# Performance work log

Measured on AMD Instinct MI355X. Metric: run time of the kernel, lower is better.

Reference implementation:

```python
import jax, jax.numpy as jnp
import numpy as np

B, C, H, W = 8, 512, 64, 128
K = 19          # num_classes
BH, BW = 2, 4   # bin_size
N = BH * BW     # bin_num
CI = C // 2     # feat_inner


def setup_inputs() -> dict:
    ks = jax.random.split(jax.random.key(0), 10)
    def nrm(k, shape, s=0.02):
        return jax.random.normal(k, shape, jnp.float32) * s
    return {
        "x": jax.random.normal(ks[0], (B, C, H, W), jnp.float32),
        "conv_cam_w": nrm(ks[1], (K, C)),
        "conv_cam_b": jnp.zeros((K,), jnp.float32),
        "gcn_w1": nrm(ks[2], (N, N), 0.1),
        "gcn_a": jnp.full((N,), 0.25, jnp.float32),
        "gcn_w2": nrm(ks[3], (C, C)),
        "fuse_w": nrm(ks[4], (1, N), 0.1),
        "fuse_b": jnp.zeros((1,), jnp.float32),
        "relu_a": jnp.full((1,), 0.25, jnp.float32),
        "q_w": nrm(ks[5], (CI, C)),
        "q_b": jnp.zeros((CI,), jnp.float32),
        "k_w": nrm(ks[6], (CI, C)),
        "k_b": jnp.zeros((CI,), jnp.float32),
        "v_w": nrm(ks[7], (CI, C)),
        "v_b": jnp.zeros((CI,), jnp.float32),
        "out_w": nrm(ks[8], (C, CI)),
        "bn_gamma": jnp.ones((C,), jnp.float32),
        "bn_beta": jnp.zeros((C,), jnp.float32),
        "out_a": jnp.full((C,), 0.25, jnp.float32),
    }


def _prelu(x, a):
    return jnp.maximum(x, 0) + a * jnp.minimum(x, 0)


def _split(t):
    # [b, cc, H, W] -> [b, N, rh*rw, cc]  (patch_split)
    b, cc = t.shape[0], t.shape[1]
    rh, rw = H // BH, W // BW
    t = t.reshape(b, cc, BH, rh, BW, rw).transpose(0, 2, 4, 3, 5, 1)
    return t.reshape(b, N, rh * rw, cc)


def _caam(x, conv_cam_w, conv_cam_b, gcn_w1, gcn_a, gcn_w2, fuse_w, fuse_b,
          relu_a, q_w, q_b, k_w, k_b, v_w, v_b, out_w, bn_gamma, bn_beta, out_a):
    b = x.shape[0]
    rh, rw = H // BH, W // BW
    # CAM (1x1 conv) + adaptive avg pool to bins + sigmoid
    cam = jnp.einsum('bchw,kc->bkhw', x, conv_cam_w) + conv_cam_b[None, :, None, None]
    cls_score = jax.nn.sigmoid(cam.reshape(b, K, BH, rh, BW, rw).mean((3, 5)))  # [b,K,BH,BW]
    cam_p = _split(cam)   # [b,N,P,K]
    x_p = _split(x)       # [b,N,P,C]
    bin_conf = cls_score.reshape(b, K, N).transpose(0, 2, 1)[..., None]  # [b,N,K,1]
    pix_conf = jax.nn.softmax(cam_p, axis=2)
    local = jnp.einsum('bnpk,bnpc->bnkc', pix_conf, x_p) * bin_conf  # [b,N,K,C]
    # GCN: conv1 over bin dim, PReLU(residual), Linear over channels
    t = jnp.einsum('nm,bmkc->bnkc', gcn_w1, local)
    t = _prelu(t + local, gcn_a[None, :, None, None])
    local = jnp.einsum('bnkc,dc->bnkd', t, gcn_w2)
    # fuse bins -> single global descriptor, PReLU(1)
    glob = jnp.einsum('on,bnkc->bokc', fuse_w, local) + fuse_b[None, :, None, None]  # [b,1,K,C]
    glob = _prelu(glob[:, 0], relu_a[0])  # [b,K,C]
    # QKV attention over bins (key/value over K class slots)
    q = jnp.einsum('bnpc,ic->bnpi', x_p, q_w) + q_b       # [b,N,P,CI]
    key = jnp.einsum('bnkc,ic->bnki', local, k_w) + k_b   # [b,N,K,CI]
    val = jnp.einsum('bkc,ic->bki', glob, v_w) + v_b      # [b,K,CI] (shared across bins)
    aff = jax.nn.softmax(jnp.einsum('bnpi,bnki->bnpk', q, key), axis=-1)
    out = jnp.einsum('bnpk,bki->bnpi', aff, val)          # [b,N,P,CI]
    # patch_recover -> [b,CI,H,W]
    out = out.reshape(b, BH, BW, rh, rw, CI).transpose(0, 5, 1, 3, 2, 4).reshape(b, CI, H, W)
    # conv_out: 1x1 conv (no bias) + BatchNorm2d (batch stats) + PReLU(C)
    y = jnp.einsum('bihw,ci->bchw', out, out_w)
    mu = y.mean((0, 2, 3), keepdims=True)
    var = y.var((0, 2, 3), keepdims=True)
    y = (y - mu) * jax.lax.rsqrt(var + 1e-5)
    y = y * bn_gamma[None, :, None, None] + bn_beta[None, :, None, None]
    y = _prelu(y, out_a[None, :, None, None])
    return x + y


def reference(x, conv_cam_w, conv_cam_b, gcn_w1, gcn_a, gcn_w2, fuse_w, fuse_b,
              relu_a, q_w, q_b, k_w, k_b, v_w, v_b, out_w, bn_gamma, bn_beta, out_a):
    return _caam(x, conv_cam_w, conv_cam_b, gcn_w1, gcn_a, gcn_w2, fuse_w, fuse_b,
                 relu_a, q_w, q_b, k_w, k_b, v_w, v_b, out_w, bn_gamma, bn_beta, out_a)
```

## Files before the change

### kernel.cpp

```cpp
#include <hip/hip_runtime.h>
#include <cstdint>
#include <cstddef>

#define B_ 8
#define C_ 512
#define H_ 64
#define W_ 128
#define HW_ 8192
#define K_ 19
#define N_ 8
#define P_ 1024
#define CI_ 256

typedef unsigned short u16;
typedef unsigned int u32;
typedef __attribute__((ext_vector_type(8))) short bf16x8;
typedef __attribute__((ext_vector_type(4))) float f32x4;

__device__ __forceinline__ u16 f2bf(float f) {
  u32 u = __float_as_uint(f);
  u32 r = (u + 0x7FFFu + ((u >> 16) & 1u)) >> 16;
  return (u16)r;
}
__device__ __forceinline__ float bf2f(u16 h) {
  return __uint_as_float(((u32)h) << 16);
}

__device__ __forceinline__ float blockSum256(float v, float* red4) {
#pragma unroll
  for (int o = 32; o > 0; o >>= 1) v += __shfl_down(v, o, 64);
  __syncthreads();
  if ((threadIdx.x & 63) == 0) red4[threadIdx.x >> 6] = v;
  __syncthreads();
  return red4[0] + red4[1] + red4[2] + red4[3];
}

__device__ __forceinline__ float blockMax256(float v, float* red4) {
#pragma unroll
  for (int o = 32; o > 0; o >>= 1) v = fmaxf(v, __shfl_down(v, o, 64));
  __syncthreads();
  if ((threadIdx.x & 63) == 0) red4[threadIdx.x >> 6] = v;
  __syncthreads();
  return fmaxf(fmaxf(red4[0], red4[1]), fmaxf(red4[2], red4[3]));
}

__device__ __forceinline__ void cvt4(const float* __restrict__ s, u16* __restrict__ d, int i) {
  float4 v = *(const float4*)&s[(size_t)i * 4];
  ushort4 o;
  o.x = f2bf(v.x); o.y = f2bf(v.y); o.z = f2bf(v.z); o.w = f2bf(v.w);
  *(ushort4*)&d[(size_t)i * 4] = o;
}

__global__ __launch_bounds__(256) void prep_kernel(const float* __restrict__ qw,
                                                   const float* __restrict__ ow,
                                                   const float* __restrict__ kw,
                                                   const float* __restrict__ gw2,
                                                   const float* __restrict__ camw,
                                                   u16* __restrict__ qwbf,
                                                   u16* __restrict__ owbf,
                                                   u16* __restrict__ kwbf,
                                                   u16* __restrict__ gw2bf,
                                                   u16* __restrict__ camwbf,
                                                   float* __restrict__ sums,
                                                   float* __restrict__ tpad) {
  int bid = blockIdx.x, tid = threadIdx.x;
  if (bid < 128) {
    cvt4(qw, qwbf, bid * 256 + tid);
  } else if (bid < 256) {
    cvt4(ow, owbf, (bid - 128) * 256 + tid);
  } else if (bid < 384) {
    cvt4(kw, kwbf, (bid - 256) * 256 + tid);
  } else if (bid < 640) {
    cvt4(gw2, gw2bf, (bid - 384) * 256 + tid);
  } else if (bid < 656) {
    int i = (bid - 640) * 256 + tid;
    if (i * 4 < K_ * C_) {
      cvt4(camw, camwbf, i);
    } else {
      ushort4 z; z.x = 0; z.y = 0; z.z = 0; z.w = 0;
      *(ushort4*)&camwbf[(size_t)i * 4] = z;
    }
  } else if (bid == 656) {
    float4 z; z.x = 0.f; z.y = 0.f; z.z = 0.f; z.w = 0.f;
    *(float4*)&sums[tid * 4] = z;
  } else {
    int i = (bid - 657) * 256 + tid;
    float4 z; z.x = 0.f; z.y = 0.f; z.z = 0.f; z.w = 0.f;
    *(float4*)&tpad[(size_t)i * 4] = z;
  }
}

__global__ __launch_bounds__(256) void xpose_kernel(const float* __restrict__ x,
                                                    u16* __restrict__ xt) {
  __shared__ float tile[64][65];
  int bid = blockIdx.x;
  int hw0 = (bid & 127) << 6;
  int c0 = ((bid >> 7) & 7) << 6;
  int b = bid >> 10;
  int tid = threadIdx.x;
  int r = tid >> 4;
  int col4 = (tid & 15) << 2;
  const float* xb = x + ((size_t)b * C_ + c0) * HW_ + hw0;
#pragma unroll
  for (int it = 0; it < 4; it++) {
    int rr = r + it * 16;
    float4 v = *(const float4*)&xb[(size_t)rr * HW_ + col4];
    tile[rr][col4 + 0] = v.x;
    tile[rr][col4 + 1] = v.y;
    tile[rr][col4 + 2] = v.z;
    tile[rr][col4 + 3] = v.w;
  }
  __syncthreads();
  u16* xo = xt + ((size_t)b * HW_ + hw0) * C_ + c0;
#pragma unroll
  for (int it = 0; it < 4; it++) {
    int hwr = r + it * 16;
    ushort4 o;
    o.x = f2bf(tile[col4 + 0][hwr]);
    o.y = f2bf(tile[col4 + 1][hwr]);
    o.z = f2bf(tile[col4 + 2][hwr]);
    o.w = f2bf(tile[col4 + 3][hwr]);
    *(ushort4*)&xo[(size_t)hwr * C_ + col4] = o;
  }
}

__global__ __launch_bounds__(256) void gemm_cam_kernel(const u16* __restrict__ A,
                                                       const u16* __restrict__ Bw,
                                                       const float* __restrict__ bias,
                                                       float* __restrict__ cam) {
  __shared__ u16 As[128 * 72];
  __shared__ u16 Bs[32 * 72];
  int b = blockIdx.y;
  int m0 = blockIdx.x * 128;
  int tid = threadIdx.x;
  int wave = tid >> 6, lane = tid & 63;
  int wm = wave * 32;
  int quad = lane >> 4, l16 = lane & 15;
  const u16* Ab = A + (size_t)b * HW_ * C_ + (size_t)m0 * C_;
  f32x4 acc[2][2] = {};
  int sr = tid >> 3;
  int sk = (tid & 7) * 8;
  for (int k0 = 0; k0 < C_; k0 += 64) {
    __syncthreads();
#pragma unroll
    for (int it = 0; it < 4; it++) {
      int r = sr + it * 32;
      *(uint4*)&As[r * 72 + sk] = *(const uint4*)&Ab[(size_t)r * C_ + k0 + sk];
    }
    { int r = tid >> 3;
      *(uint4*)&Bs[r * 72 + sk] = *(const uint4*)&Bw[(size_t)r * C_ + k0 + sk]; }
    __syncthreads();
#pragma unroll
    for (int kk = 0; kk < 2; kk++) {
      bf16x8 af[2], bfv[2];
#pragma unroll
      for (int t = 0; t < 2; t++) {
        af[t] = *(const bf16x8*)&As[(wm + t * 16 + l16) * 72 + kk * 32 + quad * 8];
        bfv[t] = *(const bf16x8*)&Bs[(t * 16 + l16) * 72 + kk * 32 + quad * 8];
      }
#pragma unroll
      for (int tm = 0; tm < 2; tm++)
#pragma unroll
        for (int tn = 0; tn < 2; tn++)
          acc[tm][tn] = __builtin_amdgcn_mfma_f32_16x16x32_bf16(af[tm], bfv[tn], acc[tm][tn], 0, 0, 0);
    }
  }
  float* C = cam + (size_t)b * K_ * HW_;
#pragma unroll
  for (int tm = 0; tm < 2; tm++) {
    int mm = m0 + wm + tm * 16 + quad * 4;
#pragma unroll
    for (int tn = 0; tn < 2; tn++) {
      int nn = tn * 16 + l16;
      if (nn < K_) {
        float bv = bias[nn];
        f32x4 v = acc[tm][tn];
        v[0] += bv; v[1] += bv; v[2] += bv; v[3] += bv;
        *(f32x4*)&C[(size_t)nn * HW_ + mm] = v;
      }
    }
  }
}

__global__ __launch_bounds__(256) void softcls_kernel(const float* __restrict__ cam,
                                                      float* __restrict__ bconf,
                                                      float* __restrict__ pconf) {
  __shared__ float red4[4];
  int bid = blockIdx.x;
  int k = bid % 19;
  int n = (bid / 19) & 7;
  int b = bid / 152;
  int bh = n >> 2, bw = n & 3;
  const float* base = cam + ((size_t)b * K_ + k) * HW_ + (bh * 32) * W_ + bw * 32;
  float v[4];
  float s = 0.f, mx = -1e30f;
#pragma unroll
  for (int j = 0; j < 4; j++) {
    int p = threadIdx.x + j * 256;
    v[j] = base[(p >> 5) * W_ + (p & 31)];
    s += v[j];
    mx = fmaxf(mx, v[j]);
  }
  float tot = blockSum256(s, red4);
  if (threadIdx.x == 0) {
    float m = tot * (1.f / 1024.f);
    bconf[bid] = 1.f / (1.f + __expf(-m));
  }
  mx = blockMax256(mx, red4);
  float e[4];
  float se = 0.f;
#pragma unroll
  for (int j = 0; j < 4; j++) { e[j] = __expf(v[j] - mx); se += e[j]; }
  se = blockSum256(se, red4);
  float inv = 1.f / se;
  float* outp = pconf + (size_t)bid * P_;
#pragma unroll
  for (int j = 0; j < 4; j++) outp[threadIdx.x + j * 256] = e[j] * inv;
}

__global__ __launch_bounds__(256) void local_part_kernel(const u16* __restrict__ xt,
                                                         const float* __restrict__ pconf,
                                                         float* __restrict__ part) {
  __shared__ __align__(16) float pcl[19 * 256];
  int bid = blockIdx.x;
  int pq = bid & 3;
  int half = (bid >> 2) & 1;
  int n = (bid >> 3) & 7;
  int b = bid >> 6;
  int tid = threadIdx.x;
  int c = half * 256 + tid;
  int bh = n >> 2, bw = n & 3;
  const float* pcb = pconf + (size_t)((b * N_ + n) * K_) * P_ + pq * 256;
  for (int e = tid; e < 19 * 64; e += 256) {
    int k = e >> 6, q4 = e & 63;
    *(float4*)&pcl[k * 256 + q4 * 4] = *(const float4*)&pcb[(size_t)k * P_ + q4 * 4];
  }
  __syncthreads();
  float acc[K_];
#pragma unroll
  for (int k = 0; k < K_; k++) acc[k] = 0.f;
  const u16* xb = xt + (size_t)b * HW_ * C_ + c;
  for (int pl0 = 0; pl0 < 256; pl0 += 8) {
    float xv[8];
#pragma unroll
    for (int g = 0; g < 2; g++) {
      int p = pq * 256 + pl0 + g * 4;
      int hw = (bh * 32 + (p >> 5)) * W_ + bw * 32 + (p & 31);
      const u16* xr = xb + (size_t)hw * C_;
#pragma unroll
      for (int j = 0; j < 4; j++) xv[g * 4 + j] = bf2f(xr[(size_t)j * C_]);
    }
#pragma unroll
    for (int k = 0; k < K_; k++) {
      float4 p0 = *(const float4*)&pcl[k * 256 + pl0];
      float4 p1 = *(const float4*)&pcl[k * 256 + pl0 + 4];
      acc[k] += p0.x * xv[0] + p0.y * xv[1] + p0.z * xv[2] + p0.w * xv[3]
              + p1.x * xv[4] + p1.y * xv[5] + p1.z * xv[6] + p1.w * xv[7];
    }
  }
  int row = (b * N_ + n) * K_;
  float* pp = part + ((size_t)pq * 1216 + row) * C_ + c;
#pragma unroll
  for (int k = 0; k < K_; k++) pp[(size_t)k * C_] = acc[k];
}

__global__ __launch_bounds__(256) void t_kernel(const float* __restrict__ part,
                                                const float* __restrict__ bconf,
                                                const float* __restrict__ gw1,
                                                const float* __restrict__ ga,
                                                u16* __restrict__ tbuf) {
  __shared__ float gw1l[64];
  __shared__ float gal[8];
  __shared__ float bcl[8];
  int tid = threadIdx.x;
  int bid = blockIdx.x;
  int half = bid & 1;
  int rem = bid >> 1;
  int k = rem % 19;
  int b = rem / 19;
  if (tid < 64) gw1l[tid] = gw1[tid];
  if (tid < 8) {
    gal[tid] = ga[tid];
    bcl[tid] = bconf[(size_t)(b * 8 + tid) * 19 + k];
  }
  __syncthreads();
  int c = half * 256 + tid;
  float lm[8];
#pragma unroll
  for (int m = 0; m < 8; m++) {
    size_t off = ((size_t)(b * N_ + m) * K_ + k) * C_ + c;
    lm[m] = (part[off] + part[off + (size_t)1216 * 512] +
             part[off + (size_t)2 * 1216 * 512] + part[off + (size_t)3 * 1216 * 512]) * bcl[m];
  }
#pragma unroll
  for (int n = 0; n < 8; n++) {
    float v = lm[n];
#pragma unroll
    for (int m = 0; m < 8; m++) v += gw1l[n * 8 + m] * lm[m];
    float t = fmaxf(v, 0.f) + gal[n] * fminf(v, 0.f);
    tbuf[((size_t)((b * N_ + n) * K_ + k)) * C_ + c] = f2bf(t);
  }
}

template <int KDIM, int NDIM, bool BIAS>
__global__ __launch_bounds__(256) void gemm_small_kernel(const u16* __restrict__ A,
                                                         const u16* __restrict__ Bw,
                                                         const float* __restrict__ bias,
                                                         float* __restrict__ f32out,
                                                         u16* __restrict__ bf16out) {
  __shared__ u16 As[128 * 72];
  __shared__ u16 Bs[128 * 72];
  constexpr int NT = NDIM / 128;
  int m0 = (blockIdx.x / NT) * 128;
  int n0 = (blockIdx.x % NT) * 128;
  int tid = threadIdx.x;
  int wave = tid >> 6, lane = tid & 63;
  int wm = (wave >> 1) * 64, wn = (wave & 1) * 64;
  int quad = lane >> 4, l16 = lane & 15;
  const u16* Ab = A + (size_t)m0 * KDIM;
  const u16* Bb = Bw + (size_t)n0 * KDIM;
  f32x4 acc[4][4] = {};
  int sr = tid >> 3;
  int sk = (tid & 7) * 8;
  for (int k0 = 0; k0 < KDIM; k0 += 64) {
    __syncthreads();
#pragma unroll
    for (int it = 0; it < 4; it++) {
      int r = sr + it * 32;
      *(uint4*)&As[r * 72 + sk] = *(const uint4*)&Ab[(size_t)r * KDIM + k0 + sk];
      *(uint4*)&Bs[r * 72 + sk] = *(const uint4*)&Bb[(size_t)r * KDIM + k0 + sk];
    }
    __syncthreads();
#pragma unroll
    for (int kk = 0; kk < 2; kk++) {
      bf16x8 af[4], bfv[4];
#pragma unroll
      for (int t = 0; t < 4; t++) {
        af[t] = *(const bf16x8*)&As[(wm + t * 16 + l16) * 72 + kk * 32 + quad * 8];
        bfv[t] = *(const bf16x8*)&Bs[(wn + t * 16 + l16) * 72 + kk * 32 + quad * 8];
      }
#pragma unroll
      for (int tm = 0; tm < 4; tm++)
#pragma unroll
        for (int tn = 0; tn < 4; tn++)
          acc[tm][tn] = __builtin_amdgcn_mfma_f32_16x16x32_bf16(af[tm], bfv[tn], acc[tm][tn], 0, 0, 0);
    }
  }
  float bv[4];
#pragma unroll
  for (int tn = 0; tn < 4; tn++)
    bv[tn] = BIAS ? bias[n0 + wn + tn * 16 + l16] : 0.f;
#pragma unroll
  for (int tm = 0; tm < 4; tm++) {
    int mm = m0 + wm + tm * 16 + quad * 4;
#pragma unroll
    for (int tn = 0; tn < 4; tn++) {
      int nn = n0 + wn + tn * 16 + l16;
#pragma unroll
      for (int reg = 0; reg < 4; reg++) {
        float v = acc[tm][tn][reg] + bv[tn];
        if (f32out) f32out[(size_t)(mm + reg) * NDIM + nn] = v;
        if (bf16out) bf16out[(size_t)(mm + reg) * NDIM + nn] = f2bf(v);
      }
    }
  }
}

__global__ __launch_bounds__(256) void glob_val_kernel(const float* __restrict__ locl2,
                                                       const float* __restrict__ fw,
                                                       const float* __restrict__ fb,
                                                       const float* __restrict__ ra,
                                                       const float* __restrict__ vw,
                                                       const float* __restrict__ vb,
                                                       float* __restrict__ valo) {
  __shared__ __align__(16) float gl[512];
  int bid = blockIdx.x;
  int k = bid % 19;
  int b = bid / 19;
  int tid = threadIdx.x;
  float fwr[8];
#pragma unroll
  for (int m = 0; m < 8; m++) fwr[m] = fw[m];
  float fbv = fb[0], rav = ra[0];
  const float* lb = locl2 + ((size_t)(b * N_) * K_ + k) * C_;
  for (int c = tid; c < C_; c += 256) {
    float v = fbv;
#pragma unroll
    for (int m = 0; m < 8; m++) v += fwr[m] * lb[(size_t)m * K_ * C_ + c];
    gl[c] = fmaxf(v, 0.f) + rav * fminf(v, 0.f);
  }
  __syncthreads();
  int i = tid;
  const float* wr = vw + (size_t)i * C_;
  float s = vb[i];
  for (int c4 = 0; c4 < C_; c4 += 4) {
    float4 wv = *(const float4*)&wr[c4];
    float4 tv = *(const float4*)&gl[c4];
    s += wv.x * tv.x + wv.y * tv.y + wv.z * tv.z + wv.w * tv.w;
  }
  valo[(size_t)bid * CI_ + i] = s;
}

template <int KDIM, int NDIM, bool TRANS_OUT, bool BIAS, bool OUTBF16, bool BNSTAT>
__global__ __launch_bounds__(256) void gemm_big_kernel(const u16* __restrict__ A,
                                                       const u16* __restrict__ Bw,
                                                       const float* __restrict__ bias,
                                                       void* __restrict__ Cout,
                                                       float* __restrict__ sums,
                                                       float* __restrict__ sumsq) {
  __shared__ u16 As[128 * 72];
  __shared__ u16 Bs[128 * 72];
  constexpr int NT = NDIM / 128;
  int b = blockIdx.y;
  int d = blockIdx.x;
  int xcd = d & 7;
  int j = d >> 3;
  int m0 = (xcd + 8 * (j / NT)) * 128;
  int n0 = (j % NT) * 128;
  int tid = threadIdx.x;
  int wave = tid >> 6, lane = tid & 63;
  int wm = (wave >> 1) * 64, wn = (wave & 1) * 64;
  int quad = lane >> 4, l16 = lane & 15;
  const u16* Ab = A + (size_t)b * 8192 * KDIM + (size_t)m0 * KDIM;
  const u16* Bb = Bw + (size_t)n0 * KDIM;
  f32x4 acc[4][4] = {};
  int sr = tid >> 3;
  int sk = (tid & 7) * 8;
  for (int k0 = 0; k0 < KDIM; k0 += 64) {
    __syncthreads();
#pragma unroll
    for (int it = 0; it < 4; it++) {
      int r = sr + it * 32;
      *(uint4*)&As[r * 72 + sk] = *(const uint4*)&Ab[(size_t)r * KDIM + k0 + sk];
      *(uint4*)&Bs[r * 72 + sk] = *(const uint4*)&Bb[(size_t)r * KDIM + k0 + sk];
    }
    __syncthreads();
#pragma unroll
    for (int kk = 0; kk < 2; kk++) {
      bf16x8 af[4], bfv[4];
#pragma unroll
      for (int t = 0; t < 4; t++) {
        af[t] = *(const bf16x8*)&As[(wm + t * 16 + l16) * 72 + kk * 32 + quad * 8];
        bfv[t] = *(const bf16x8*)&Bs[(wn + t * 16 + l16) * 72 + kk * 32 + quad * 8];
      }
#pragma unroll
      for (int tm = 0; tm < 4; tm++)
#pragma unroll
        for (int tn = 0; tn < 4; tn++)
          acc[tm][tn] = __builtin_amdgcn_mfma_f32_16x16x32_bf16(af[tm], bfv[tn], acc[tm][tn], 0, 0, 0);
    }
  }
  if constexpr (!TRANS_OUT) {
    float bv[4];
#pragma unroll
    for (int tn = 0; tn < 4; tn++)
      bv[tn] = BIAS ? bias[n0 + wn + tn * 16 + l16] : 0.f;
#pragma unroll
    for (int tm = 0; tm < 4; tm++) {
      int mm = m0 + wm + tm * 16 + quad * 4;
#pragma unroll
      for (int tn = 0; tn < 4; tn++) {
        int nn = n0 + wn + tn * 16 + l16;
        if constexpr (OUTBF16) {
          u16* C = (u16*)Cout + (size_t)b * 8192 * NDIM;
#pragma unroll
          for (int reg = 0; reg < 4; reg++)
            C[(size_t)(mm + reg) * NDIM + nn] = f2bf(acc[tm][tn][reg] + bv[tn]);
        } else {
          float* C = (float*)Cout + (size_t)b * 8192 * NDIM;
#pragma unroll
          for (int reg = 0; reg < 4; reg++)
            C[(size_t)(mm + reg) * NDIM + nn] = acc[tm][tn][reg] + bv[tn];
        }
      }
    }
  } else {
    float* C = (float*)Cout + (size_t)b * NDIM * 8192;
#pragma unroll
    for (int tm = 0; tm < 4; tm++) {
      int mm = m0 + wm + tm * 16 + quad * 4;
#pragma unroll
      for (int tn = 0; tn < 4; tn++) {
        int nn = n0 + wn + tn * 16 + l16;
        *(f32x4*)&C[(size_t)nn * 8192 + mm] = acc[tm][tn];
      }
    }
    if constexpr (BNSTAT) {
#pragma unroll
      for (int tn = 0; tn < 4; tn++) {
        int nn = n0 + wn + tn * 16 + l16;
        float s = 0.f, q = 0.f;
#pragma unroll
        for (int tm = 0; tm < 4; tm++)
#pragma unroll
          for (int reg = 0; reg < 4; reg++) {
            float v = acc[tm][tn][reg];
            s += v;
            q += v * v;
          }
        s += __shfl_xor(s, 16, 64); q += __shfl_xor(q, 16, 64);
        s += __shfl_xor(s, 32, 64); q += __shfl_xor(q, 32, 64);
        if (quad == 0) {
          atomicAdd(&sums[nn], s);
          atomicAdd(&sumsq[nn], q);
        }
      }
    }
  }
}

__global__ __launch_bounds__(256) void attn2_kernel(const u16* __restrict__ q,
                                                    const float* __restrict__ keyo,
                                                    const float* __restrict__ valo,
                                                    u16* __restrict__ obuf) {
  __shared__ float keyl[19 * 256];
  __shared__ float vall[19 * 256];
  __shared__ float aff[128 * 20];
  int bid = blockIdx.x;
  int rg = bid & 7;
  int n = (bid >> 3) & 7;
  int b = bid >> 6;
  int bh = n >> 2, bw = n & 3;
  int tid = threadIdx.x;
  const float* ksrc = keyo + (size_t)((b * 8 + n) * 19) * 256;
  for (int e = tid; e < 19 * 256; e += 256) keyl[e] = ksrc[e];
  __syncthreads();
  if (tid < 128) {
    int r = rg * 4 + (tid >> 5);
    int wc = tid & 31;
    int hw = (bh * 32 + r) * W_ + bw * 32 + wc;
    const u16* qr = q + ((size_t)b * HW_ + hw) * 256;
    float acc[19];
#pragma unroll
    for (int k = 0; k < 19; k++) acc[k] = 0.f;
    for (int i0 = 0; i0 < 256; i0 += 8) {
      uint4 v = *(const uint4*)&qr[i0];
      float f0 = __uint_as_float((v.x & 0xFFFFu) << 16);
      float f1 = __uint_as_float(v.x & 0xFFFF0000u);
      float f2 = __uint_as_float((v.y & 0xFFFFu) << 16);
      float f3 = __uint_as_float(v.y & 0xFFFF0000u);
      float f4 = __uint_as_float((v.z & 0xFFFFu) << 16);
      float f5 = __uint_as_float(v.z & 0xFFFF0000u);
      float f6 = __uint_as_float((v.w & 0xFFFFu) << 16);
      float f7 = __uint_as_float(v.w & 0xFFFF0000u);
#pragma unroll
      for (int k = 0; k < 19; k++) {
        const float* kr = &keyl[k * 256 + i0];
        acc[k] += f0 * kr[0] + f1 * kr[1] + f2 * kr[2] + f3 * kr[3] +
                  f4 * kr[4] + f5 * kr[5] + f6 * kr[6] + f7 * kr[7];
      }
    }
    float mx = -1e30f;
#pragma unroll
    for (int k = 0; k < 19; k++) mx = fmaxf(mx, acc[k]);
    float se = 0.f;
#pragma unroll
    for (int k = 0; k < 19; k++) { acc[k] = __expf(acc[k] - mx); se += acc[k]; }
    float inv = 1.f / se;
#pragma unroll
    for (int k = 0; k < 19; k++) aff[tid * 20 + k] = acc[k] * inv;
  } else {
    const float* vsrc = valo + (size_t)b * 19 * 256;
    for (int e = tid - 128; e < 19 * 256; e += 128) vall[e] = vsrc[e];
  }
  __syncthreads();
  int px = tid & 127;
  int ih = (tid >> 7) * 128;
  int r3 = rg * 4 + (px >> 5);
  int wc3 = px & 31;
  int hw3 = (bh * 32 + r3) * W_ + bw * 32 + wc3;
  float av[19];
#pragma unroll
  for (int k = 0; k < 19; k++) av[k] = aff[px * 20 + k];
  u16* ob = obuf + ((size_t)b * HW_ + hw3) * 256 + ih;
  for (int i0 = 0; i0 < 128; i0 += 16) {
    float o16[16];
#pragma unroll
    for (int j = 0; j < 16; j++) o16[j] = 0.f;
#pragma unroll
    for (int k = 0; k < 19; k++) {
      float a = av[k];
      const float* vr = &vall[k * 256 + ih + i0];
#pragma unroll
      for (int j = 0; j < 16; j++) o16[j] += a * vr[j];
    }
    uint4 w0, w1;
    w0.x = (u32)f2bf(o16[0]) | ((u32)f2bf(o16[1]) << 16);
    w0.y = (u32)f2bf(o16[2]) | ((u32)f2bf(o16[3]) << 16);
    w0.z = (u32)f2bf(o16[4]) | ((u32)f2bf(o16[5]) << 16);
    w0.w = (u32)f2bf(o16[6]) | ((u32)f2bf(o16[7]) << 16);
    w1.x = (u32)f2bf(o16[8]) | ((u32)f2bf(o16[9]) << 16);
    w1.y = (u32)f2bf(o16[10]) | ((u32)f2bf(o16[11]) << 16);
    w1.z = (u32)f2bf(o16[12]) | ((u32)f2bf(o16[13]) << 16);
    w1.w = (u32)f2bf(o16[14]) | ((u32)f2bf(o16[15]) << 16);
    *(uint4*)&ob[i0] = w0;
    *(uint4*)&ob[i0 + 8] = w1;
  }
}

__global__ __launch_bounds__(512) void bnfinal_kernel(const float* __restrict__ sums,
                                                      const float* __restrict__ sumsq,
                                                      const float* __restrict__ gamma,
                                                      const float* __restrict__ beta,
                                                      float* __restrict__ scale,
                                                      float* __restrict__ shift) {
  int c = threadIdx.x;
  const float inv_cnt = 1.f / 65536.f;
  float mu = sums[c] * inv_cnt;
  float var = sumsq[c] * inv_cnt - mu * mu;
  float iv = rsqrtf(var + 1e-5f);
  float sc = gamma[c] * iv;
  scale[c] = sc;
  shift[c] = beta[c] - mu * sc;
}

__global__ __launch_bounds__(256) void final_kernel(const float* __restrict__ x,
                                                    const float* __restrict__ scale,
                                                    const float* __restrict__ shift,
                                                    const float* __restrict__ oa,
                                                    float* __restrict__ out) {
  size_t base = (size_t)blockIdx.x * 4096 + threadIdx.x * 4;
  int c = (int)((base >> 13) & 511);
  float sc = scale[c], sh = shift[c], a = oa[c];
#pragma unroll
  for (int jj = 0; jj < 4; jj++) {
    size_t idx = base + (size_t)jj * 1024;
    float4 y = *(float4*)&out[idx];
    float4 xv = *(const float4*)&x[idx];
    float4 r;
    float t;
    t = y.x * sc + sh; r.x = xv.x + fmaxf(t, 0.f) + a * fminf(t, 0.f);
    t = y.y * sc + sh; r.y = xv.y + fmaxf(t, 0.f) + a * fminf(t, 0.f);
    t = y.z * sc + sh; r.z = xv.z + fmaxf(t, 0.f) + a * fminf(t, 0.f);
    t = y.w * sc + sh; r.w = xv.w + fmaxf(t, 0.f) + a * fminf(t, 0.f);
    *(float4*)&out[idx] = r;
  }
}

extern "C" void kernel_launch(void* const* d_in, const int* in_sizes, int n_in,
                              void* d_out, int out_size, void* d_ws, size_t ws_size,
                              hipStream_t stream) {
  const float* x     = (const float*)d_in[0];
  const float* camw  = (const float*)d_in[1];
  const float* camb  = (const float*)d_in[2];
  const float* gw1   = (const float*)d_in[3];
  const float* ga    = (const float*)d_in[4];
  const float* gw2   = (const float*)d_in[5];
  const float* fw    = (const float*)d_in[6];
  const float* fb    = (const float*)d_in[7];
  const float* ra    = (const float*)d_in[8];
  const float* qw    = (const float*)d_in[9];
  const float* qb    = (const float*)d_in[10];
  const float* kw    = (const float*)d_in[11];
  const float* kb    = (const float*)d_in[12];
  const float* vw    = (const float*)d_in[13];
  const float* vb    = (const float*)d_in[14];
  const float* ow    = (const float*)d_in[15];
  const float* gamma = (const float*)d_in[16];
  const float* beta  = (const float*)d_in[17];
  const float* oa    = (const float*)d_in[18];
  float* out = (float*)d_out;
  float* ws = (float*)d_ws;

  float* cam    = ws;
  float* bconf  = cam + 1245184;
  float* pconf  = bconf + 2048;
  float* locl   = pconf + 1245184;
  float* locl2f = locl + 622592;
  float* keyo   = locl2f + 655360;
  float* valo   = keyo + 327680;
  float* sums   = valo + 38912;
  float* sumsq  = sums + 512;
  float* scale  = sumsq + 512;
  float* shift  = scale + 512;
  u16* qwbf   = (u16*)(shift + 512);
  u16* owbf   = qwbf + 131072;
  u16* kwbf   = owbf + 131072;
  u16* gw2bf  = kwbf + 131072;
  u16* camwbf = gw2bf + 262144;
  u16* tbuf   = camwbf + 16384;
  u16* l2bf   = tbuf + 655360;
  u16* xt     = l2bf + 655360;
  u16* obuf   = xt;
  u16* qbuf   = xt + 33554432;
  float* part = (float*)qbuf;

  prep_kernel<<<673, 256, 0, stream>>>(qw, ow, kw, gw2, camw,
                                       qwbf, owbf, kwbf, gw2bf, camwbf,
                                       sums, (float*)(tbuf + 1216 * 512));
  xpose_kernel<<<8192, 256, 0, stream>>>(x, xt);
  gemm_cam_kernel<<<dim3(64, 8), 256, 0, stream>>>(xt, camwbf, camb, cam);
  softcls_kernel<<<1216, 256, 0, stream>>>(cam, bconf, pconf);
  local_part_kernel<<<512, 256, 0, stream>>>(xt, pconf, part);
  t_kernel<<<304, 256, 0, stream>>>(part, bconf, gw1, ga, tbuf);
  gemm_small_kernel<512, 512, false>
      <<<40, 256, 0, stream>>>(tbuf, gw2bf, nullptr, locl2f, l2bf);
  gemm_small_kernel<512, 256, true>
      <<<20, 256, 0, stream>>>(l2bf, kwbf, kb, keyo, nullptr);
  glob_val_kernel<<<152, 256, 0, stream>>>(locl2f, fw, fb, ra, vw, vb, valo);
  gemm_big_kernel<512, 256, false, true, true, false>
      <<<dim3(128, 8), 256, 0, stream>>>(xt, qwbf, qb, qbuf, nullptr, nullptr);
  attn2_kernel<<<512, 256, 0, stream>>>(qbuf, keyo, valo, obuf);
  gemm_big_kernel<256, 512, true, false, false, true>
      <<<dim3(256, 8), 256, 0, stream>>>(obuf, owbf, nullptr, out, sums, sumsq);
  bnfinal_kernel<<<1, 512, 0, stream>>>(sums, sumsq, gamma, beta, scale, shift);
  final_kernel<<<8192, 256, 0, stream>>>(x, scale, shift, oa, out);
}
```

Baseline: 569.2 us.

## Use direct global-to-LDS loads with XOR swizzle and merge small kernels

Result: faster. 549.3 us (-3.5%).

```diff
diff --git a/kernel.cpp b/kernel.cpp
--- a/kernel.cpp
+++ b/kernel.cpp
@@ -26,6 +26,33 @@
   return __uint_as_float(((u32)h) << 16);
 }
 
+__device__ __forceinline__ void gload16(const u16* g, u16* l) {
+  __builtin_amdgcn_global_load_lds(
+      (const __attribute__((address_space(1))) unsigned int*)g,
+      (__attribute__((address_space(3))) unsigned int*)l, 16, 0, 0);
+}
+
+__device__ __forceinline__ void stage128(const u16* __restrict__ src, size_t ld, int k0,
+                                         u16* lds, int wave, int lane) {
+  int rsub = lane >> 3;
+  int swz = ((lane & 7) ^ rsub) << 3;
+#pragma unroll
+  for (int i = 0; i < 4; i++) {
+    int rowbase = wave * 8 + i * 32;
+    gload16(src + (size_t)(rowbase + rsub) * ld + k0 + swz, lds + rowbase * 64);
+  }
+}
+__device__ __forceinline__ void stage32(const u16* __restrict__ src, size_t ld, int k0,
+                                        u16* lds, int wave, int lane) {
+  int rsub = lane >> 3;
+  int swz = ((lane & 7) ^ rsub) << 3;
+  int rowbase = wave * 8;
+  gload16(src + (size_t)(rowbase + rsub) * ld + k0 + swz, lds + rowbase * 64);
+}
+__device__ __forceinline__ bf16x8 frag(const u16* lds, int row, int qbyte) {
+  return *(const bf16x8*)((const char*)lds + row * 128 + (qbyte ^ ((row & 7) << 4)));
+}
+
 __device__ __forceinline__ float blockSum256(float v, float* red4) {
 #pragma unroll
   for (int o = 32; o > 0; o >>= 1) v += __shfl_down(v, o, 64);
@@ -51,53 +78,54 @@
   *(ushort4*)&d[(size_t)i * 4] = o;
 }
 
-__global__ __launch_bounds__(256) void prep_kernel(const float* __restrict__ qw,
-                                                   const float* __restrict__ ow,
-                                                   const float* __restrict__ kw,
-                                                   const float* __restrict__ gw2,
-                                                   const float* __restrict__ camw,
-                                                   u16* __restrict__ qwbf,
-                                                   u16* __restrict__ owbf,
-                                                   u16* __restrict__ kwbf,
-                                                   u16* __restrict__ gw2bf,
-                                                   u16* __restrict__ camwbf,
-                                                   float* __restrict__ sums,
-                                                   float* __restrict__ tpad) {
-  int bid = blockIdx.x, tid = threadIdx.x;
-  if (bid < 128) {
-    cvt4(qw, qwbf, bid * 256 + tid);
-  } else if (bid < 256) {
-    cvt4(ow, owbf, (bid - 128) * 256 + tid);
-  } else if (bid < 384) {
-    cvt4(kw, kwbf, (bid - 256) * 256 + tid);
-  } else if (bid < 640) {
-    cvt4(gw2, gw2bf, (bid - 384) * 256 + tid);
-  } else if (bid < 656) {
-    int i = (bid - 640) * 256 + tid;
-    if (i * 4 < K_ * C_) {
-      cvt4(camw, camwbf, i);
-    } else {
-      ushort4 z; z.x = 0; z.y = 0; z.z = 0; z.w = 0;
-      *(ushort4*)&camwbf[(size_t)i * 4] = z;
-    }
-  } else if (bid == 656) {
-    float4 z; z.x = 0.f; z.y = 0.f; z.z = 0.f; z.w = 0.f;
-    *(float4*)&sums[tid * 4] = z;
-  } else {
-    int i = (bid - 657) * 256 + tid;
-    float4 z; z.x = 0.f; z.y = 0.f; z.z = 0.f; z.w = 0.f;
-    *(float4*)&tpad[(size_t)i * 4] = z;
-  }
-}
-
-__global__ __launch_bounds__(256) void xpose_kernel(const float* __restrict__ x,
-                                                    u16* __restrict__ xt) {
+__global__ __launch_bounds__(256) void xpose_prep_kernel(const float* __restrict__ x,
+                                                         u16* __restrict__ xt,
+                                                         const float* __restrict__ qw,
+                                                         const float* __restrict__ ow,
+                                                         const float* __restrict__ kw,
+                                                         const float* __restrict__ gw2,
+                                                         const float* __restrict__ camw,
+                                                         u16* __restrict__ qwbf,
+                                                         u16* __restrict__ owbf,
+                                                         u16* __restrict__ kwbf,
+                                                         u16* __restrict__ gw2bf,
+                                                         u16* __restrict__ camwbf,
+                                                         float* __restrict__ sums,
+                                                         float* __restrict__ tpad) {
   __shared__ float tile[64][65];
   int bid = blockIdx.x;
+  int tid = threadIdx.x;
+  if (bid >= 8192) {
+    int pb = bid - 8192;
+    if (pb < 128) {
+      cvt4(qw, qwbf, pb * 256 + tid);
+    } else if (pb < 256) {
+      cvt4(ow, owbf, (pb - 128) * 256 + tid);
+    } else if (pb < 384) {
+      cvt4(kw, kwbf, (pb - 256) * 256 + tid);
+    } else if (pb < 640) {
+      cvt4(gw2, gw2bf, (pb - 384) * 256 + tid);
+    } else if (pb < 656) {
+      int i = (pb - 640) * 256 + tid;
+      if (i * 4 < K_ * C_) {
+        cvt4(camw, camwbf, i);
+      } else {
+        ushort4 z; z.x = 0; z.y = 0; z.z = 0; z.w = 0;
+        *(ushort4*)&camwbf[(size_t)i * 4] = z;
+      }
+    } else if (pb == 656) {
+      float4 z; z.x = 0.f; z.y = 0.f; z.z = 0.f; z.w = 0.f;
+      *(float4*)&sums[tid * 4] = z;
+    } else {
+      int i = (pb - 657) * 256 + tid;
+      float4 z; z.x = 0.f; z.y = 0.f; z.z = 0.f; z.w = 0.f;
+      *(float4*)&tpad[(size_t)i * 4] = z;
+    }
+    return;
+  }
   int hw0 = (bid & 127) << 6;
   int c0 = ((bid >> 7) & 7) << 6;
   int b = bid >> 10;
-  int tid = threadIdx.x;
   int r = tid >> 4;
   int col4 = (tid & 15) << 2;
   const float* xb = x + ((size_t)b * C_ + c0) * HW_ + hw0;
@@ -128,8 +156,8 @@
                                                        const u16* __restrict__ Bw,
                                                        const float* __restrict__ bias,
                                                        float* __restrict__ cam) {
-  __shared__ u16 As[128 * 72];
-  __shared__ u16 Bs[32 * 72];
+  __shared__ __align__(16) u16 As[128 * 64];
+  __shared__ __align__(16) u16 Bs[32 * 64];
   int b = blockIdx.y;
   int m0 = blockIdx.x * 128;
   int tid = threadIdx.x;
@@ -138,25 +166,19 @@
   int quad = lane >> 4, l16 = lane & 15;
   const u16* Ab = A + (size_t)b * HW_ * C_ + (size_t)m0 * C_;
   f32x4 acc[2][2] = {};
-  int sr = tid >> 3;
-  int sk = (tid & 7) * 8;
   for (int k0 = 0; k0 < C_; k0 += 64) {
     __syncthreads();
-#pragma unroll
-    for (int it = 0; it < 4; it++) {
-      int r = sr + it * 32;
-      *(uint4*)&As[r * 72 + sk] = *(const uint4*)&Ab[(size_t)r * C_ + k0 + sk];
-    }
-    { int r = tid >> 3;
-      *(uint4*)&Bs[r * 72 + sk] = *(const uint4*)&Bw[(size_t)r * C_ + k0 + sk]; }
+    stage128(Ab, C_, k0, As, wave, lane);
+    stage32(Bw, C_, k0, Bs, wave, lane);
     __syncthreads();
 #pragma unroll
     for (int kk = 0; kk < 2; kk++) {
+      int qb_ = kk * 64 + quad * 16;
       bf16x8 af[2], bfv[2];
 #pragma unroll
       for (int t = 0; t < 2; t++) {
-        af[t] = *(const bf16x8*)&As[(wm + t * 16 + l16) * 72 + kk * 32 + quad * 8];
-        bfv[t] = *(const bf16x8*)&Bs[(t * 16 + l16) * 72 + kk * 32 + quad * 8];
+        af[t] = frag(As, wm + t * 16 + l16, qb_);
+        bfv[t] = frag(Bs, t * 16 + l16, qb_);
       }
 #pragma unroll
       for (int tm = 0; tm < 2; tm++)
@@ -303,16 +325,16 @@
 }
 
 template <int KDIM, int NDIM, bool BIAS>
-__global__ __launch_bounds__(256) void gemm_small_kernel(const u16* __restrict__ A,
-                                                         const u16* __restrict__ Bw,
-                                                         const float* __restrict__ bias,
-                                                         float* __restrict__ f32out,
-                                                         u16* __restrict__ bf16out) {
-  __shared__ u16 As[128 * 72];
-  __shared__ u16 Bs[128 * 72];
+__device__ __forceinline__ void gemm_small_body(int bidx,
+                                                const u16* __restrict__ A,
+                                                const u16* __restrict__ Bw,
+                                                const float* __restrict__ bias,
+                                                float* __restrict__ f32out,
+                                                u16* __restrict__ bf16out,
+                                                u16* As, u16* Bs) {
   constexpr int NT = NDIM / 128;
-  int m0 = (blockIdx.x / NT) * 128;
-  int n0 = (blockIdx.x % NT) * 128;
+  int m0 = (bidx / NT) * 128;
+  int n0 = (bidx % NT) * 128;
   int tid = threadIdx.x;
   int wave = tid >> 6, lane = tid & 63;
   int wm = (wave >> 1) * 64, wn = (wave & 1) * 64;
@@ -320,24 +342,19 @@
   const u16* Ab = A + (size_t)m0 * KDIM;
   const u16* Bb = Bw + (size_t)n0 * KDIM;
   f32x4 acc[4][4] = {};
-  int sr = tid >> 3;
-  int sk = (tid & 7) * 8;
   for (int k0 = 0; k0 < KDIM; k0 += 64) {
     __syncthreads();
-#pragma unroll
-    for (int it = 0; it < 4; it++) {
-      int r = sr + it * 32;
-      *(uint4*)&As[r * 72 + sk] = *(const uint4*)&Ab[(size_t)r * KDIM + k0 + sk];
-      *(uint4*)&Bs[r * 72 + sk] = *(const uint4*)&Bb[(size_t)r * KDIM + k0 + sk];
-    }
+    stage128(Ab, KDIM, k0, As, wave, lane);
+    stage128(Bb, KDIM, k0, Bs, wave, lane);
     __syncthreads();
 #pragma unroll
     for (int kk = 0; kk < 2; kk++) {
+      int qb_ = kk * 64 + quad * 16;
       bf16x8 af[4], bfv[4];
 #pragma unroll
       for (int t = 0; t < 4; t++) {
-        af[t] = *(const bf16x8*)&As[(wm + t * 16 + l16) * 72 + kk * 32 + quad * 8];
-        bfv[t] = *(const bf16x8*)&Bs[(wn + t * 16 + l16) * 72 + kk * 32 + quad * 8];
+        af[t] = frag(As, wm + t * 16 + l16, qb_);
+        bfv[t] = frag(Bs, wn + t * 16 + l16, qb_);
       }
 #pragma unroll
       for (int tm = 0; tm < 4; tm++)
@@ -366,15 +383,26 @@
   }
 }
 
-__global__ __launch_bounds__(256) void glob_val_kernel(const float* __restrict__ locl2,
-                                                       const float* __restrict__ fw,
-                                                       const float* __restrict__ fb,
-                                                       const float* __restrict__ ra,
-                                                       const float* __restrict__ vw,
-                                                       const float* __restrict__ vb,
-                                                       float* __restrict__ valo) {
-  __shared__ __align__(16) float gl[512];
-  int bid = blockIdx.x;
+template <int KDIM, int NDIM, bool BIAS>
+__global__ __launch_bounds__(256) void gemm_small_kernel(const u16* __restrict__ A,
+                                                         const u16* __restrict__ Bw,
+                                                         const float* __restrict__ bias,
+                                                         float* __restrict__ f32out,
+                                                         u16* __restrict__ bf16out) {
+  __shared__ __align__(16) u16 As[128 * 64];
+  __shared__ __align__(16) u16 Bs[128 * 64];
+  gemm_small_body<KDIM, NDIM, BIAS>(blockIdx.x, A, Bw, bias, f32out, bf16out, As, Bs);
+}
+
+__device__ __forceinline__ void glob_val_body(int bid,
+                                              const float* __restrict__ locl2,
+                                              const float* __restrict__ fw,
+                                              const float* __restrict__ fb,
+                                              const float* __restrict__ ra,
+                                              const float* __restrict__ vw,
+                                              const float* __restrict__ vb,
+                                              float* __restrict__ valo,
+                                              float* gl) {
   int k = bid % 19;
   int b = bid / 19;
   int tid = threadIdx.x;
@@ -401,6 +429,26 @@
   valo[(size_t)bid * CI_ + i] = s;
 }
 
+__global__ __launch_bounds__(256) void small2_globval_kernel(const u16* __restrict__ A,
+                                                             const u16* __restrict__ Bw,
+                                                             const float* __restrict__ bias,
+                                                             float* __restrict__ keyo,
+                                                             const float* __restrict__ locl2,
+                                                             const float* __restrict__ fw,
+                                                             const float* __restrict__ fb,
+                                                             const float* __restrict__ ra,
+                                                             const float* __restrict__ vw,
+                                                             const float* __restrict__ vb,
+                                                             float* __restrict__ valo) {
+  __shared__ __align__(16) u16 As[128 * 64];
+  __shared__ __align__(16) u16 Bs[128 * 64];
+  if (blockIdx.x < 20) {
+    gemm_small_body<512, 256, true>(blockIdx.x, A, Bw, bias, keyo, nullptr, As, Bs);
+  } else {
+    glob_val_body(blockIdx.x - 20, locl2, fw, fb, ra, vw, vb, valo, (float*)As);
+  }
+}
+
 template <int KDIM, int NDIM, bool TRANS_OUT, bool BIAS, bool OUTBF16, bool BNSTAT>
 __global__ __launch_bounds__(256) void gemm_big_kernel(const u16* __restrict__ A,
                                                        const u16* __restrict__ Bw,
@@ -408,8 +456,8 @@
                                                        void* __restrict__ Cout,
                                                        float* __restrict__ sums,
                                                        float* __restrict__ sumsq) {
-  __shared__ u16 As[128 * 72];
-  __shared__ u16 Bs[128 * 72];
+  __shared__ __align__(16) u16 As[128 * 64];
+  __shared__ __align__(16) u16 Bs[128 * 64];
   constexpr int NT = NDIM / 128;
   int b = blockIdx.y;
   int d = blockIdx.x;
@@ -424,24 +472,19 @@
   const u16* Ab = A + (size_t)b * 8192 * KDIM + (size_t)m0 * KDIM;
   const u16* Bb = Bw + (size_t)n0 * KDIM;
   f32x4 acc[4][4] = {};
-  int sr = tid >> 3;
-  int sk = (tid & 7) * 8;
   for (int k0 = 0; k0 < KDIM; k0 += 64) {
     __syncthreads();
-#pragma unroll
-    for (int it = 0; it < 4; it++) {
-      int r = sr + it * 32;
-      *(uint4*)&As[r * 72 + sk] = *(const uint4*)&Ab[(size_t)r * KDIM + k0 + sk];
-      *(uint4*)&Bs[r * 72 + sk] = *(const uint4*)&Bb[(size_t)r * KDIM + k0 + sk];
-    }
+    stage128(Ab, KDIM, k0, As, wave, lane);
+    stage128(Bb, KDIM, k0, Bs, wave, lane);
     __syncthreads();
 #pragma unroll
     for (int kk = 0; kk < 2; kk++) {
+      int qb_ = kk * 64 + quad * 16;
       bf16x8 af[4], bfv[4];
 #pragma unroll
       for (int t = 0; t < 4; t++) {
-        af[t] = *(const bf16x8*)&As[(wm + t * 16 + l16) * 72 + kk * 32 + quad * 8];
-        bfv[t] = *(const bf16x8*)&Bs[(wn + t * 16 + l16) * 72 + kk * 32 + quad * 8];
+        af[t] = frag(As, wm + t * 16 + l16, qb_);
+        bfv[t] = frag(Bs, wn + t * 16 + l16, qb_);
       }
 #pragma unroll
       for (int tm = 0; tm < 4; tm++)
@@ -598,30 +641,22 @@
   }
 }
 
-__global__ __launch_bounds__(512) void bnfinal_kernel(const float* __restrict__ sums,
-                                                      const float* __restrict__ sumsq,
-                                                      const float* __restrict__ gamma,
-                                                      const float* __restrict__ beta,
-                                                      float* __restrict__ scale,
-                                                      float* __restrict__ shift) {
-  int c = threadIdx.x;
+__global__ __launch_bounds__(256) void final_kernel(const float* __restrict__ x,
+                                                    const float* __restrict__ sums,
+                                                    const float* __restrict__ sumsq,
+                                                    const float* __restrict__ gamma,
+                                                    const float* __restrict__ beta,
+                                                    const float* __restrict__ oa,
+                                                    float* __restrict__ out) {
+  size_t base = (size_t)blockIdx.x * 4096 + threadIdx.x * 4;
+  int c = (int)((base >> 13) & 511);
   const float inv_cnt = 1.f / 65536.f;
   float mu = sums[c] * inv_cnt;
   float var = sumsq[c] * inv_cnt - mu * mu;
   float iv = rsqrtf(var + 1e-5f);
   float sc = gamma[c] * iv;
-  scale[c] = sc;
-  shift[c] = beta[c] - mu * sc;
-}
-
-__global__ __launch_bounds__(256) void final_kernel(const float* __restrict__ x,
-                                                    const float* __restrict__ scale,
-                                                    const float* __restrict__ shift,
-                                                    const float* __restrict__ oa,
-                                                    float* __restrict__ out) {
-  size_t base = (size_t)blockIdx.x * 4096 + threadIdx.x * 4;
-  int c = (int)((base >> 13) & 511);
-  float sc = scale[c], sh = shift[c], a = oa[c];
+  float sh = beta[c] - mu * sc;
+  float a = oa[c];
 #pragma unroll
   for (int jj = 0; jj < 4; jj++) {
     size_t idx = base + (size_t)jj * 1024;
@@ -685,24 +720,21 @@
   u16* qbuf   = xt + 33554432;
   float* part = (float*)qbuf;
 
-  prep_kernel<<<673, 256, 0, stream>>>(qw, ow, kw, gw2, camw,
-                                       qwbf, owbf, kwbf, gw2bf, camwbf,
-                                       sums, (float*)(tbuf + 1216 * 512));
-  xpose_kernel<<<8192, 256, 0, stream>>>(x, xt);
+  xpose_prep_kernel<<<8865, 256, 0, stream>>>(x, xt, qw, ow, kw, gw2, camw,
+                                              qwbf, owbf, kwbf, gw2bf, camwbf,
+                                              sums, (float*)(tbuf + 1216 * 512));
   gemm_cam_kernel<<<dim3(64, 8), 256, 0, stream>>>(xt, camwbf, camb, cam);
   softcls_kernel<<<1216, 256, 0, stream>>>(cam, bconf, pconf);
   local_part_kernel<<<512, 256, 0, stream>>>(xt, pconf, part);
   t_kernel<<<304, 256, 0, stream>>>(part, bconf, gw1, ga, tbuf);
   gemm_small_kernel<512, 512, false>
       <<<40, 256, 0, stream>>>(tbuf, gw2bf, nullptr, locl2f, l2bf);
-  gemm_small_kernel<512, 256, true>
-      <<<20, 256, 0, stream>>>(l2bf, kwbf, kb, keyo, nullptr);
-  glob_val_kernel<<<152, 256, 0, stream>>>(locl2f, fw, fb, ra, vw, vb, valo);
+  small2_globval_kernel<<<172, 256, 0, stream>>>(l2bf, kwbf, kb, keyo,
+                                                 locl2f, fw, fb, ra, vw, vb, valo);
   gemm_big_kernel<512, 256, false, true, true, false>
       <<<dim3(128, 8), 256, 0, stream>>>(xt, qwbf, qb, qbuf, nullptr, nullptr);
   attn2_kernel<<<512, 256, 0, stream>>>(qbuf, keyo, valo, obuf);
   gemm_big_kernel<256, 512, true, false, false, true>
       <<<dim3(256, 8), 256, 0, stream>>>(obuf, owbf, nullptr, out, sums, sumsq);
-  bnfinal_kernel<<<1, 512, 0, stream>>>(sums, sumsq, gamma, beta, scale, shift);
-  final_kernel<<<8192, 256, 0, stream>>>(x, scale, shift, oa, out);
-}
+  final_kernel<<<8192, 256, 0, stream>>>(x, sums, sumsq, gamma, beta, oa, out);
+}
```
